# Kernel optimization log

Measured on AMD Instinct MI355X. Metric: run time of the kernel, lower is better.

The kernel has to match this reference:

```python
import jax, jax.numpy as jnp
import numpy as np

NUM_SEGMENTS = 512
N = 200000
D = 256


def setup_inputs() -> dict:
    key = jax.random.key(0)
    k = jax.random.split(key, 6)
    x = jax.random.normal(k[0], (N, D), dtype=jnp.float32)
    batch = jnp.sort(jax.random.randint(k[1], (N,), 0, NUM_SEGMENTS))
    batch = batch.at[-1].set(NUM_SEGMENTS - 1)  # ensure batch.max()+1 == NUM_SEGMENTS
    W1 = jax.random.normal(k[2], (D, D // 2), dtype=jnp.float32) * (1.0 / np.sqrt(D))
    b1 = jax.random.normal(k[3], (D // 2,), dtype=jnp.float32) * 0.01
    W2 = jax.random.normal(k[4], (D // 2, 1), dtype=jnp.float32) * (1.0 / np.sqrt(D // 2))
    b2 = jax.random.normal(k[5], (1,), dtype=jnp.float32) * 0.01
    return {"x": x, "batch": batch, "W1": W1, "b1": b1, "W2": W2, "b2": b2}


def reference(x, batch, W1, b1, W2, b2):
    # attention MLP: Linear -> Tanh -> Linear -> [N, 1]
    scores = (jnp.tanh(x @ W1 + b1) @ W2 + b2)[:, 0]  # [N]
    # segment softmax (numerically stable): subtract per-segment max
    smax = jax.ops.segment_max(scores, batch, num_segments=NUM_SEGMENTS)  # [G]
    e = jnp.exp(scores - smax[batch])  # [N]
    denom = jax.ops.segment_sum(e, batch, num_segments=NUM_SEGMENTS)  # [G]
    denom = jnp.where(denom > 0, denom, 1.0)  # guard empty segments (original yields zeros)
    w = e / denom[batch]  # [N]
    # weighted sum pooling per segment -> [G, D]
    return jax.ops.segment_sum(x * w[:, None], batch, num_segments=NUM_SEGMENTS)
```

## Files before the change

kernel.cpp:

```cpp
#include <hip/hip_runtime.h>
#include <hip/hip_bf16.h>
#include <math.h>


typedef __attribute__((ext_vector_type(4))) float f32x4;
typedef __attribute__((ext_vector_type(8))) short s16x8;
typedef __attribute__((ext_vector_type(8))) unsigned short u16x8;

#define MFMA16(A, B, C) __builtin_amdgcn_mfma_f32_16x16x32_bf16((A), (B), (C), 0, 0, 0)

__device__ __forceinline__ unsigned short f2bf_rne(float f) {
    unsigned int u = __float_as_uint(f);
    unsigned int r = u + 0x7FFFu + ((u >> 16) & 1u);
    return (unsigned short)(r >> 16);
}
__device__ __forceinline__ float bf2f(unsigned short h) {
    return __uint_as_float(((unsigned int)h) << 16);
}

__global__ __launch_bounds__(256)
void prep_w1(const float* __restrict__ W1, unsigned short* __restrict__ bh,
             unsigned short* __restrict__ bl)
{
    for (int idx = blockIdx.x * 256 + threadIdx.x; idx < 128 * 256;
         idx += gridDim.x * 256) {
        int n = idx & 127, k = idx >> 7;
        float f = W1[(size_t)k * 128 + n];
        unsigned short h = f2bf_rne(f);
        bh[(size_t)n * 256 + k] = h;
        bl[(size_t)n * 256 + k] = f2bf_rne(f - bf2f(h));
    }
}

#define LPITCH 40

__global__ __launch_bounds__(256, 3)
void scores_mfma(const float* __restrict__ x,
                 const unsigned short* __restrict__ bh,
                 const unsigned short* __restrict__ bl,
                 const float* __restrict__ b1, const float* __restrict__ W2,
                 const float* __restrict__ b2, float* __restrict__ scores, int N)
{
    __shared__ __align__(16) unsigned short Ahi[128 * LPITCH];
    __shared__ __align__(16) unsigned short Alo[128 * LPITCH];
    __shared__ __align__(16) unsigned short Bhi[128 * LPITCH];
    __shared__ __align__(16) unsigned short Blo[128 * LPITCH];

    const int tid  = threadIdx.x;
    const int wave = tid >> 6;
    const int lane = tid & 63;
    const int c    = lane & 15;
    const int q    = lane >> 4;
    const int rowBase = blockIdx.x * 128;

    f32x4 acc[2][8];
#pragma unroll
    for (int mt = 0; mt < 2; ++mt)
#pragma unroll
        for (int nt = 0; nt < 8; ++nt)
            acc[mt][nt] = (f32x4){0.f, 0.f, 0.f, 0.f};

    const int arow  = rowBase + (tid >> 1);
    const int ak16  = (tid & 1) * 16;
    const int nB    = tid & 127;
    const int bk16  = (tid >> 7) * 16;

    f32x4 pa0, pa1, pa2, pa3;
    u16x8 pb0, pb1, pl0, pl1;

    auto loadA = [&](int k0) {
        if (arow < N) {
            const float* p = x + (size_t)arow * 256 + k0 + ak16;
            pa0 = *(const f32x4*)(p);
            pa1 = *(const f32x4*)(p + 4);
            pa2 = *(const f32x4*)(p + 8);
            pa3 = *(const f32x4*)(p + 12);
        } else {
            pa0 = pa1 = pa2 = pa3 = (f32x4){0.f, 0.f, 0.f, 0.f};
        }
    };
    auto loadB = [&](int k0) {
        const size_t base = (size_t)nB * 256 + k0 + bk16;
        pb0 = *(const u16x8*)(bh + base);
        pb1 = *(const u16x8*)(bh + base + 8);
        pl0 = *(const u16x8*)(bl + base);
        pl1 = *(const u16x8*)(bl + base + 8);
    };

    loadA(0);
    loadB(0);

    for (int it = 0; it < 8; ++it) {
        float af[16];
        *(f32x4*)&af[0]  = pa0; *(f32x4*)&af[4]  = pa1;
        *(f32x4*)&af[8]  = pa2; *(f32x4*)&af[12] = pa3;
        unsigned short ah[16], al[16];
#pragma unroll
        for (int j = 0; j < 8; ++j) {
            float a0 = af[2 * j], a1 = af[2 * j + 1];
            __hip_bfloat162 h2 = __float22bfloat162_rn(make_float2(a0, a1));
            ushort2 hu = *(ushort2*)&h2;
            float r0 = a0 - bf2f(hu.x), r1 = a1 - bf2f(hu.y);
            __hip_bfloat162 l2 = __float22bfloat162_rn(make_float2(r0, r1));
            ushort2 lu = *(ushort2*)&l2;
            ah[2 * j] = hu.x; ah[2 * j + 1] = hu.y;
            al[2 * j] = lu.x; al[2 * j + 1] = lu.y;
        }

        __syncthreads();
        {
            const int ar = tid >> 1;
            *(u16x8*)&Ahi[ar * LPITCH + ak16 + 0] = *(u16x8*)&ah[0];
            *(u16x8*)&Ahi[ar * LPITCH + ak16 + 8] = *(u16x8*)&ah[8];
            *(u16x8*)&Alo[ar * LPITCH + ak16 + 0] = *(u16x8*)&al[0];
            *(u16x8*)&Alo[ar * LPITCH + ak16 + 8] = *(u16x8*)&al[8];
            *(u16x8*)&Bhi[nB * LPITCH + bk16 + 0] = pb0;
            *(u16x8*)&Bhi[nB * LPITCH + bk16 + 8] = pb1;
            *(u16x8*)&Blo[nB * LPITCH + bk16 + 0] = pl0;
            *(u16x8*)&Blo[nB * LPITCH + bk16 + 8] = pl1;
        }
        __syncthreads();

        if (it < 7) {
            loadA((it + 1) * 32);
            loadB((it + 1) * 32);
        }

        s16x8 fah[2], fal[2];
#pragma unroll
        for (int mt = 0; mt < 2; ++mt) {
            int m = wave * 32 + mt * 16 + c;
            fah[mt] = *(const s16x8*)&Ahi[m * LPITCH + q * 8];
            fal[mt] = *(const s16x8*)&Alo[m * LPITCH + q * 8];
        }
#pragma unroll
        for (int nt = 0; nt < 8; ++nt) {
            int nr = nt * 16 + c;
            s16x8 fbh = *(const s16x8*)&Bhi[nr * LPITCH + q * 8];
            s16x8 fbl = *(const s16x8*)&Blo[nr * LPITCH + q * 8];
#pragma unroll
            for (int mt = 0; mt < 2; ++mt) {
                acc[mt][nt] = MFMA16(fah[mt], fbh, acc[mt][nt]);
                acc[mt][nt] = MFMA16(fah[mt], fbl, acc[mt][nt]);
                acc[mt][nt] = MFMA16(fal[mt], fbh, acc[mt][nt]);
            }
        }
    }

    float b1v[8], w2v[8];
#pragma unroll
    for (int nt = 0; nt < 8; ++nt) {
        b1v[nt] = b1[nt * 16 + c];
        w2v[nt] = W2[nt * 16 + c];
    }
    const float bias2 = b2[0];

#pragma unroll
    for (int mt = 0; mt < 2; ++mt) {
#pragma unroll
        for (int reg = 0; reg < 4; ++reg) {
            float p = 0.f;
#pragma unroll
            for (int nt = 0; nt < 8; ++nt) {
                float v = acc[mt][nt][reg] + b1v[nt];
                float e = __expf(2.f * v);
                p += (1.f - 2.f / (e + 1.f)) * w2v[nt];
            }
#pragma unroll
            for (int off = 8; off > 0; off >>= 1)
                p += __shfl_xor(p, off, 16);
            if (c == 0) {
                int row = rowBase + wave * 32 + mt * 16 + q * 4 + reg;
                if (row < N) scores[row] = p + bias2;
            }
        }
    }
}

__device__ __forceinline__ int lower_bound_dev(const int* __restrict__ b, int n, int v)
{
    int lo = 0, hi = n;
    while (lo < hi) {
        int mid = (lo + hi) >> 1;
        if (b[mid] < v) lo = mid + 1; else hi = mid;
    }
    return lo;
}

__global__ __launch_bounds__(1024)
void segpool_kernel(const float* __restrict__ x, const int* __restrict__ batch,
                    const float* __restrict__ scores, float* __restrict__ out, int N)
{
    const int g = blockIdx.x;
    const int tid = threadIdx.x;
    const int fidx  = tid & 63;
    const int rslot = tid >> 6;

    __shared__ int se[2];
    __shared__ float sred[1024];
    __shared__ float4 rbuf[16][64];

    if (tid < 2) se[tid] = lower_bound_dev(batch, N, g + tid);
    __syncthreads();
    const int start = se[0], end = se[1];

    float m = -INFINITY;
    for (int i = start + tid; i < end; i += 1024) m = fmaxf(m, scores[i]);
#pragma unroll
    for (int off = 32; off > 0; off >>= 1) m = fmaxf(m, __shfl_xor(m, off, 64));
    if ((tid & 63) == 0) sred[tid >> 6] = m;
    __syncthreads();
    if (tid < 16) {
        float v = sred[tid];
#pragma unroll
        for (int off = 8; off > 0; off >>= 1) v = fmaxf(v, __shfl_xor(v, off, 16));
        if (tid == 0) sred[0] = v;
    }
    __syncthreads();
    m = sred[0];
    __syncthreads();

    float ssum = 0.f;
    for (int i = start + tid; i < end; i += 1024) ssum += expf(scores[i] - m);
#pragma unroll
    for (int off = 32; off > 0; off >>= 1) ssum += __shfl_xor(ssum, off, 64);
    if ((tid & 63) == 0) sred[tid >> 6] = ssum;
    __syncthreads();
    if (tid < 16) {
        float v = sred[tid];
#pragma unroll
        for (int off = 8; off > 0; off >>= 1) v += __shfl_xor(v, off, 16);
        if (tid == 0) sred[0] = v;
    }
    __syncthreads();
    const float denom = sred[0];
    const float inv = (denom > 0.f) ? 1.f / denom : 0.f;

    float4 acc = make_float4(0.f, 0.f, 0.f, 0.f);
    for (int base = start; base < end; base += 1024) {
        int cnt = min(1024, end - base);
        __syncthreads();
        if (tid < cnt) sred[tid] = expf(scores[base + tid] - m) * inv;
        __syncthreads();
#pragma unroll 2
        for (int j = rslot; j < cnt; j += 16) {
            float w = sred[j];
            float4 v = *(const float4*)(x + (size_t)(base + j) * 256 + fidx * 4);
            acc.x = fmaf(w, v.x, acc.x);
            acc.y = fmaf(w, v.y, acc.y);
            acc.z = fmaf(w, v.z, acc.z);
            acc.w = fmaf(w, v.w, acc.w);
        }
    }

    rbuf[rslot][fidx] = acc;
    __syncthreads();
#pragma unroll
    for (int s = 8; s > 0; s >>= 1) {
        if (rslot < s) {
            float4 o = rbuf[rslot + s][fidx];
            acc.x += o.x; acc.y += o.y; acc.z += o.z; acc.w += o.w;
            rbuf[rslot][fidx] = acc;
        }
        __syncthreads();
    }
    if (rslot == 0)
        ((float4*)out)[(size_t)g * 64 + fidx] = acc;
}

extern "C" void kernel_launch(void* const* d_in, const int* in_sizes, int n_in,
                              void* d_out, int out_size, void* d_ws, size_t ws_size,
                              hipStream_t stream) {
    const float* x     = (const float*)d_in[0];
    const int*   batch = (const int*)  d_in[1];
    const float* W1    = (const float*)d_in[2];
    const float* b1    = (const float*)d_in[3];
    const float* W2    = (const float*)d_in[4];
    const float* b2    = (const float*)d_in[5];
    float* out = (float*)d_out;

    const int N = in_sizes[1];
    const int G = out_size / 256;

    float* scores = (float*)d_ws;

    unsigned short* bh = (unsigned short*)d_out;
    unsigned short* bl = bh + 128 * 256;

    prep_w1<<<64, 256, 0, stream>>>(W1, bh, bl);
    const int mblocks = (N + 127) / 128;
    scores_mfma<<<mblocks, 256, 0, stream>>>(x, bh, bl, b1, W2, b2, scores, N);
    segpool_kernel<<<G, 1024, 0, stream>>>(x, batch, scores, out, N);
}
```

Baseline: 360.3 us.

## Drop LDS staging in score GEMM and split pooling into row-parallel atomics

The score GEMM now loads x and the split-bf16 W1 fragments straight from global memory into MFMA operands, with no LDS staging and no block barriers, and the occupancy hint rises to 4. Segment softmax moves into a separate stats kernel that writes normalized weights in place. Pooling becomes a row-parallel kernel over 256-row chunks that flushes per-segment partial sums with atomicAdd into a pre-zeroed output. This is meant to fix load imbalance and low parallelism in the old one-block-per-segment pooling, at the cost of atomics, extra launches, and redundant global W1 reads per wave.

```diff
diff --git a/kernel.cpp b/kernel.cpp
--- a/kernel.cpp
+++ b/kernel.cpp
@@ -16,6 +16,13 @@
 }
 __device__ __forceinline__ float bf2f(unsigned short h) {
     return __uint_as_float(((unsigned int)h) << 16);
+}
+
+__global__ __launch_bounds__(256)
+void zero_out(float* __restrict__ out, int n)
+{
+    int i = blockIdx.x * 256 + threadIdx.x;
+    if (i < n) out[i] = 0.f;
 }
 
 __global__ __launch_bounds__(256)
@@ -32,26 +39,19 @@
     }
 }
 
-#define LPITCH 40
-
-__global__ __launch_bounds__(256, 3)
+__global__ __launch_bounds__(256, 4)
 void scores_mfma(const float* __restrict__ x,
                  const unsigned short* __restrict__ bh,
                  const unsigned short* __restrict__ bl,
                  const float* __restrict__ b1, const float* __restrict__ W2,
                  const float* __restrict__ b2, float* __restrict__ scores, int N)
 {
-    __shared__ __align__(16) unsigned short Ahi[128 * LPITCH];
-    __shared__ __align__(16) unsigned short Alo[128 * LPITCH];
-    __shared__ __align__(16) unsigned short Bhi[128 * LPITCH];
-    __shared__ __align__(16) unsigned short Blo[128 * LPITCH];
-
     const int tid  = threadIdx.x;
     const int wave = tid >> 6;
     const int lane = tid & 63;
     const int c    = lane & 15;
     const int q    = lane >> 4;
-    const int rowBase = blockIdx.x * 128;
+    const int rowBase = blockIdx.x * 128 + wave * 32;
 
     f32x4 acc[2][8];
 #pragma unroll
@@ -60,84 +60,44 @@
         for (int nt = 0; nt < 8; ++nt)
             acc[mt][nt] = (f32x4){0.f, 0.f, 0.f, 0.f};
 
-    const int arow  = rowBase + (tid >> 1);
-    const int ak16  = (tid & 1) * 16;
-    const int nB    = tid & 127;
-    const int bk16  = (tid >> 7) * 16;
-
-    f32x4 pa0, pa1, pa2, pa3;
-    u16x8 pb0, pb1, pl0, pl1;
-
-    auto loadA = [&](int k0) {
-        if (arow < N) {
-            const float* p = x + (size_t)arow * 256 + k0 + ak16;
-            pa0 = *(const f32x4*)(p);
-            pa1 = *(const f32x4*)(p + 4);
-            pa2 = *(const f32x4*)(p + 8);
-            pa3 = *(const f32x4*)(p + 12);
-        } else {
-            pa0 = pa1 = pa2 = pa3 = (f32x4){0.f, 0.f, 0.f, 0.f};
-        }
-    };
-    auto loadB = [&](int k0) {
-        const size_t base = (size_t)nB * 256 + k0 + bk16;
-        pb0 = *(const u16x8*)(bh + base);
-        pb1 = *(const u16x8*)(bh + base + 8);
-        pl0 = *(const u16x8*)(bl + base);
-        pl1 = *(const u16x8*)(bl + base + 8);
-    };
-
-    loadA(0);
-    loadB(0);
-
-    for (int it = 0; it < 8; ++it) {
-        float af[16];
-        *(f32x4*)&af[0]  = pa0; *(f32x4*)&af[4]  = pa1;
-        *(f32x4*)&af[8]  = pa2; *(f32x4*)&af[12] = pa3;
-        unsigned short ah[16], al[16];
-#pragma unroll
-        for (int j = 0; j < 8; ++j) {
-            float a0 = af[2 * j], a1 = af[2 * j + 1];
-            __hip_bfloat162 h2 = __float22bfloat162_rn(make_float2(a0, a1));
-            ushort2 hu = *(ushort2*)&h2;
-            float r0 = a0 - bf2f(hu.x), r1 = a1 - bf2f(hu.y);
-            __hip_bfloat162 l2 = __float22bfloat162_rn(make_float2(r0, r1));
-            ushort2 lu = *(ushort2*)&l2;
-            ah[2 * j] = hu.x; ah[2 * j + 1] = hu.y;
-            al[2 * j] = lu.x; al[2 * j + 1] = lu.y;
-        }
-
-        __syncthreads();
-        {
-            const int ar = tid >> 1;
-            *(u16x8*)&Ahi[ar * LPITCH + ak16 + 0] = *(u16x8*)&ah[0];
-            *(u16x8*)&Ahi[ar * LPITCH + ak16 + 8] = *(u16x8*)&ah[8];
-            *(u16x8*)&Alo[ar * LPITCH + ak16 + 0] = *(u16x8*)&al[0];
-            *(u16x8*)&Alo[ar * LPITCH + ak16 + 8] = *(u16x8*)&al[8];
-            *(u16x8*)&Bhi[nB * LPITCH + bk16 + 0] = pb0;
-            *(u16x8*)&Bhi[nB * LPITCH + bk16 + 8] = pb1;
-            *(u16x8*)&Blo[nB * LPITCH + bk16 + 0] = pl0;
-            *(u16x8*)&Blo[nB * LPITCH + bk16 + 8] = pl1;
-        }
-        __syncthreads();
-
-        if (it < 7) {
-            loadA((it + 1) * 32);
-            loadB((it + 1) * 32);
-        }
-
+    const int r0 = rowBase + c;
+    const int r1 = rowBase + 16 + c;
+
+#pragma unroll 2
+    for (int k0 = 0; k0 < 256; k0 += 32) {
         s16x8 fah[2], fal[2];
 #pragma unroll
         for (int mt = 0; mt < 2; ++mt) {
-            int m = wave * 32 + mt * 16 + c;
-            fah[mt] = *(const s16x8*)&Ahi[m * LPITCH + q * 8];
-            fal[mt] = *(const s16x8*)&Alo[m * LPITCH + q * 8];
+            int row = mt ? r1 : r0;
+            f32x4 a0 = (f32x4){0.f, 0.f, 0.f, 0.f};
+            f32x4 a1 = (f32x4){0.f, 0.f, 0.f, 0.f};
+            if (row < N) {
+                const float* p = x + (size_t)row * 256 + k0 + q * 8;
+                a0 = *(const f32x4*)(p);
+                a1 = *(const f32x4*)(p + 4);
+            }
+            float af[8];
+            *(f32x4*)&af[0] = a0; *(f32x4*)&af[4] = a1;
+            unsigned short ah[8], al[8];
+#pragma unroll
+            for (int j = 0; j < 4; ++j) {
+                float v0 = af[2 * j], v1 = af[2 * j + 1];
+                __hip_bfloat162 h2 = __float22bfloat162_rn(make_float2(v0, v1));
+                ushort2 hu = *(ushort2*)&h2;
+                float rr0 = v0 - bf2f(hu.x), rr1 = v1 - bf2f(hu.y);
+                __hip_bfloat162 l2 = __float22bfloat162_rn(make_float2(rr0, rr1));
+                ushort2 lu = *(ushort2*)&l2;
+                ah[2 * j] = hu.x; ah[2 * j + 1] = hu.y;
+                al[2 * j] = lu.x; al[2 * j + 1] = lu.y;
+            }
+            fah[mt] = *(s16x8*)ah;
+            fal[mt] = *(s16x8*)al;
         }
 #pragma unroll
         for (int nt = 0; nt < 8; ++nt) {
-            int nr = nt * 16 + c;
-            s16x8 fbh = *(const s16x8*)&Bhi[nr * LPITCH + q * 8];
-            s16x8 fbl = *(const s16x8*)&Blo[nr * LPITCH + q * 8];
+            const size_t boff = (size_t)(nt * 16 + c) * 256 + k0 + q * 8;
+            s16x8 fbh = *(const s16x8*)(bh + boff);
+            s16x8 fbl = *(const s16x8*)(bl + boff);
 #pragma unroll
             for (int mt = 0; mt < 2; ++mt) {
                 acc[mt][nt] = MFMA16(fah[mt], fbh, acc[mt][nt]);
@@ -170,7 +130,7 @@
             for (int off = 8; off > 0; off >>= 1)
                 p += __shfl_xor(p, off, 16);
             if (c == 0) {
-                int row = rowBase + wave * 32 + mt * 16 + q * 4 + reg;
+                int row = rowBase + mt * 16 + q * 4 + reg;
                 if (row < N) scores[row] = p + bias2;
             }
         }
@@ -187,85 +147,83 @@
     return lo;
 }
 
-__global__ __launch_bounds__(1024)
-void segpool_kernel(const float* __restrict__ x, const int* __restrict__ batch,
-                    const float* __restrict__ scores, float* __restrict__ out, int N)
+__global__ __launch_bounds__(256)
+void seg_stats(const int* __restrict__ batch, float* __restrict__ sw, int N)
 {
     const int g = blockIdx.x;
     const int tid = threadIdx.x;
+    __shared__ int se[2];
+    __shared__ float red[4];
+    __shared__ float bc[2];
+
+    if (tid < 2) se[tid] = lower_bound_dev(batch, N, g + tid);
+    __syncthreads();
+    const int start = se[0], end = se[1];
+
+    float m = -INFINITY;
+    for (int i = start + tid; i < end; i += 256) m = fmaxf(m, sw[i]);
+#pragma unroll
+    for (int off = 32; off > 0; off >>= 1) m = fmaxf(m, __shfl_xor(m, off, 64));
+    if ((tid & 63) == 0) red[tid >> 6] = m;
+    __syncthreads();
+    m = fmaxf(fmaxf(red[0], red[1]), fmaxf(red[2], red[3]));
+
+    float s = 0.f;
+    for (int i = start + tid; i < end; i += 256) s += expf(sw[i] - m);
+#pragma unroll
+    for (int off = 32; off > 0; off >>= 1) s += __shfl_xor(s, off, 64);
+    __syncthreads();
+    if ((tid & 63) == 0) red[tid >> 6] = s;
+    __syncthreads();
+    if (tid == 0) {
+        float d = red[0] + red[1] + red[2] + red[3];
+        bc[0] = m;
+        bc[1] = (d > 0.f) ? 1.f / d : 0.f;
+    }
+    __syncthreads();
+    const float mm = bc[0], inv = bc[1];
+
+    for (int i = start + tid; i < end; i += 256)
+        sw[i] = expf(sw[i] - mm) * inv;
+}
+
+#define PR 256
+__global__ __launch_bounds__(1024)
+void pool_kernel(const float* __restrict__ x, const int* __restrict__ batch,
+                 const float* __restrict__ wgt, float* __restrict__ out, int N)
+{
+    const int tid   = threadIdx.x;
     const int fidx  = tid & 63;
-    const int rslot = tid >> 6;
-
-    __shared__ int se[2];
-    __shared__ float sred[1024];
-    __shared__ float4 rbuf[16][64];
-
-    if (tid < 2) se[tid] = lower_bound_dev(batch, N, g + tid);
-    __syncthreads();
-    const int start = se[0], end = se[1];
-
-    float m = -INFINITY;
-    for (int i = start + tid; i < end; i += 1024) m = fmaxf(m, scores[i]);
-#pragma unroll
-    for (int off = 32; off > 0; off >>= 1) m = fmaxf(m, __shfl_xor(m, off, 64));
-    if ((tid & 63) == 0) sred[tid >> 6] = m;
-    __syncthreads();
-    if (tid < 16) {
-        float v = sred[tid];
-#pragma unroll
-        for (int off = 8; off > 0; off >>= 1) v = fmaxf(v, __shfl_xor(v, off, 16));
-        if (tid == 0) sred[0] = v;
-    }
-    __syncthreads();
-    m = sred[0];
-    __syncthreads();
-
-    float ssum = 0.f;
-    for (int i = start + tid; i < end; i += 1024) ssum += expf(scores[i] - m);
-#pragma unroll
-    for (int off = 32; off > 0; off >>= 1) ssum += __shfl_xor(ssum, off, 64);
-    if ((tid & 63) == 0) sred[tid >> 6] = ssum;
-    __syncthreads();
-    if (tid < 16) {
-        float v = sred[tid];
-#pragma unroll
-        for (int off = 8; off > 0; off >>= 1) v += __shfl_xor(v, off, 16);
-        if (tid == 0) sred[0] = v;
-    }
-    __syncthreads();
-    const float denom = sred[0];
-    const float inv = (denom > 0.f) ? 1.f / denom : 0.f;
-
-    float4 acc = make_float4(0.f, 0.f, 0.f, 0.f);
-    for (int base = start; base < end; base += 1024) {
-        int cnt = min(1024, end - base);
-        __syncthreads();
-        if (tid < cnt) sred[tid] = expf(scores[base + tid] - m) * inv;
-        __syncthreads();
-#pragma unroll 2
-        for (int j = rslot; j < cnt; j += 16) {
-            float w = sred[j];
-            float4 v = *(const float4*)(x + (size_t)(base + j) * 256 + fidx * 4);
-            acc.x = fmaf(w, v.x, acc.x);
-            acc.y = fmaf(w, v.y, acc.y);
-            acc.z = fmaf(w, v.z, acc.z);
-            acc.w = fmaf(w, v.w, acc.w);
-        }
-    }
-
-    rbuf[rslot][fidx] = acc;
-    __syncthreads();
-#pragma unroll
-    for (int s = 8; s > 0; s >>= 1) {
-        if (rslot < s) {
-            float4 o = rbuf[rslot + s][fidx];
-            acc.x += o.x; acc.y += o.y; acc.z += o.z; acc.w += o.w;
-            rbuf[rslot][fidx] = acc;
-        }
-        __syncthreads();
-    }
-    if (rslot == 0)
-        ((float4*)out)[(size_t)g * 64 + fidx] = acc;
+    const int wv    = tid >> 6;
+    const int r0    = blockIdx.x * PR;
+    const int rend  = min(r0 + PR, N);
+
+    f32x4 acc = (f32x4){0.f, 0.f, 0.f, 0.f};
+    int seg_cur = -1;
+
+    for (int row = r0 + wv; row < rend; row += 16) {
+        int seg = batch[row];
+        if (seg != seg_cur) {
+            if (seg_cur >= 0) {
+                float* dst = out + (size_t)seg_cur * 256 + fidx * 4;
+                atomicAdd(dst + 0, acc.x); atomicAdd(dst + 1, acc.y);
+                atomicAdd(dst + 2, acc.z); atomicAdd(dst + 3, acc.w);
+            }
+            acc = (f32x4){0.f, 0.f, 0.f, 0.f};
+            seg_cur = seg;
+        }
+        float w = wgt[row];
+        f32x4 v = *(const f32x4*)(x + (size_t)row * 256 + fidx * 4);
+        acc.x = fmaf(w, v.x, acc.x);
+        acc.y = fmaf(w, v.y, acc.y);
+        acc.z = fmaf(w, v.z, acc.z);
+        acc.w = fmaf(w, v.w, acc.w);
+    }
+    if (seg_cur >= 0) {
+        float* dst = out + (size_t)seg_cur * 256 + fidx * 4;
+        atomicAdd(dst + 0, acc.x); atomicAdd(dst + 1, acc.y);
+        atomicAdd(dst + 2, acc.z); atomicAdd(dst + 3, acc.w);
+    }
 }
 
 extern "C" void kernel_launch(void* const* d_in, const int* in_sizes, int n_in,
@@ -282,13 +240,14 @@
     const int N = in_sizes[1];
     const int G = out_size / 256;
 
-    float* scores = (float*)d_ws;
-
-    unsigned short* bh = (unsigned short*)d_out;
+    float* scores      = (float*)d_ws;
+    unsigned short* bh = (unsigned short*)((char*)d_ws + (1 << 20));
     unsigned short* bl = bh + 128 * 256;
 
+    zero_out<<<(out_size + 255) / 256, 256, 0, stream>>>(out, out_size);
     prep_w1<<<64, 256, 0, stream>>>(W1, bh, bl);
     const int mblocks = (N + 127) / 128;
     scores_mfma<<<mblocks, 256, 0, stream>>>(x, bh, bl, b1, W2, b2, scores, N);
-    segpool_kernel<<<G, 1024, 0, stream>>>(x, batch, scores, out, N);
-}
+    seg_stats<<<G, 256, 0, stream>>>(batch, scores, N);
+    pool_kernel<<<(N + PR - 1) / PR, 1024, 0, stream>>>(x, batch, scores, out, N);
+}
```

Result: slower. 495.5 us (+37.5%).
